# Kernel optimization log

Hardware: AMD Instinct MI355X
Metric: run time of the kernel (lower is better)

Reference implementation:

```python
import jax, jax.numpy as jnp
import numpy as np

S, B, C = 7, 2, 1
LAMBDA_COORD, LAMBDA_NOOBJ = 5.0, 0.5
EPS = 1e-6
BATCH = 32768


def setup_inputs() -> dict:
    key = jax.random.key(0)
    k1, k2, k3, k4 = jax.random.split(key, 4)
    predictions = jax.random.normal(k1, (BATCH, S, S, B * 5 + C), dtype=jnp.float32)
    coords = jax.random.uniform(k2, (BATCH, S, S, 4), dtype=jnp.float32) * 0.9 + 0.05
    conf = jax.random.randint(k3, (BATCH, S, S, 1), 0, 2).astype(jnp.float32)  # exactly 0 or 1
    cls = jax.random.randint(k4, (BATCH, S, S, C), 0, 2).astype(jnp.float32)
    targets = jnp.concatenate([coords, conf, cls], axis=-1)  # [BATCH,S,S,6]
    return {"predictions": predictions, "targets": targets}


def reference(predictions, targets):
    dt = predictions.dtype
    obj = (targets[..., 4] == 1.0).astype(dt)      # [bs,S,S]
    noobj = (targets[..., 4] == 0.0).astype(dt)    # [bs,S,S]

    pb = predictions[..., : B * 5].reshape(predictions.shape[:-1] + (B, 5))  # [bs,S,S,B,5]
    tb = targets[..., :5]                                                    # [bs,S,S,5]

    # IoU of each of the B predicted boxes vs the target box (per cell)
    sxy = jax.nn.sigmoid(pb[..., 0:2])
    awh = jnp.abs(pb[..., 2:4])
    p1 = sxy - awh / 2
    p2 = sxy + awh / 2
    t1 = tb[..., 0:2] - tb[..., 2:4] / 2
    t2 = tb[..., 0:2] + tb[..., 2:4] / 2
    lo = jnp.maximum(p1, t1[..., None, :])
    hi = jnp.minimum(p2, t2[..., None, :])
    inter = jnp.prod(jnp.maximum(hi - lo, 0.0), axis=-1)        # [bs,S,S,B]
    parea = jnp.prod(jnp.abs(p2 - p1), axis=-1)                 # [bs,S,S,B]
    tarea = (tb[..., 2] * tb[..., 3])[..., None]
    iou = inter / (parea + tarea - inter + EPS)

    best = jnp.argmax(iou, axis=-1)                             # [bs,S,S]
    bb = jnp.take_along_axis(pb, best[..., None, None], axis=-2)[..., 0, :]  # [bs,S,S,5]

    coord = LAMBDA_COORD * jnp.sum(
        obj * jnp.sum((jax.nn.sigmoid(bb[..., 0:2]) - tb[..., 0:2]) ** 2, axis=-1)
    )
    coord = coord + LAMBDA_COORD * jnp.sum(
        obj * jnp.sum((jnp.sqrt(jnp.abs(bb[..., 2:4]) + EPS) - jnp.sqrt(tb[..., 2:4] + EPS)) ** 2, axis=-1)
    )

    conf_obj = jnp.sum(obj * (jax.nn.sigmoid(bb[..., 4]) - tb[..., 4]) ** 2)

    conf_noobj = LAMBDA_NOOBJ * jnp.sum(
        noobj[..., None] * (jax.nn.sigmoid(pb[..., 4]) - tb[..., 4:5]) ** 2
    )

    # C == 1: binary cross-entropy with logits, summed over obj cells
    pc = predictions[..., B * 5 : B * 5 + C]
    tc = targets[..., 5 : 5 + C]
    bce = jnp.maximum(pc, 0.0) - pc * tc + jnp.log1p(jnp.exp(-jnp.abs(pc)))
    class_loss = jnp.sum(obj[..., None] * bce)

    bs = predictions.shape[0]
    total = (coord + conf_obj + conf_noobj + class_loss) / bs
    return (total, coord / bs, conf_obj / bs, conf_noobj / bs, class_loss / bs)
```

## Files before the change

kernel.cpp:

```cpp
#include <hip/hip_runtime.h>
#include <math.h>


#define PRED_C 11
#define TGT_C  6
#define TPB    256
#define CELLS_PER_THREAD 2
#define LAMBDA_COORD 5.0f
#define LAMBDA_NOOBJ 0.5f
#define EPSV 1e-6f

typedef float f4u __attribute__((ext_vector_type(4), aligned(4)));
typedef float f2u __attribute__((ext_vector_type(2), aligned(4)));

__device__ __forceinline__ float fsig(float x) {
    return __builtin_amdgcn_rcpf(1.0f + __expf(-x));
}

__device__ __forceinline__ void cell_loss(f4u a, f4u b, f4u c, f4u t4, f2u t2,
                                          float& acc_coord, float& acc_cobj,
                                          float& acc_cnoobj, float& acc_cls)
{
    const float tx = t4.x, ty = t4.y, tw = t4.z, th = t4.w;
    const float tconf = t2.x, tcls = t2.y;
    const float obj   = (tconf == 1.0f) ? 1.0f : 0.0f;
    const float noobj = (tconf == 0.0f) ? 1.0f : 0.0f;

    const float t1x = tx - tw * 0.5f, t1y = ty - th * 0.5f;
    const float t2x = tx + tw * 0.5f, t2y = ty + th * 0.5f;
    const float tarea = tw * th;

    const float px[2] = { a.x, b.y };
    const float py[2] = { a.y, b.z };
    const float pw[2] = { a.z, b.w };
    const float ph[2] = { a.w, c.y };
    const float pf[2] = { b.x, c.z };

    float iou[2], sx[2], sy[2], aw[2], ah[2], scf[2];
    #pragma unroll
    for (int bb = 0; bb < 2; ++bb) {
        sx[bb]  = fsig(px[bb]);
        sy[bb]  = fsig(py[bb]);
        scf[bb] = fsig(pf[bb]);
        aw[bb]  = fabsf(pw[bb]);
        ah[bb]  = fabsf(ph[bb]);
        const float p1x = sx[bb] - aw[bb] * 0.5f, p1y = sy[bb] - ah[bb] * 0.5f;
        const float p2x = sx[bb] + aw[bb] * 0.5f, p2y = sy[bb] + ah[bb] * 0.5f;
        const float ix = fminf(p2x, t2x) - fmaxf(p1x, t1x);
        const float iy = fminf(p2y, t2y) - fmaxf(p1y, t1y);
        const float inter = fmaxf(ix, 0.0f) * fmaxf(iy, 0.0f);
        const float parea = aw[bb] * ah[bb];
        iou[bb] = inter * __builtin_amdgcn_rcpf(parea + tarea - inter + EPSV);
    }
    const int best = (iou[1] > iou[0]) ? 1 : 0;

    const float dx = sx[best] - tx;
    const float dy = sy[best] - ty;
    const float dw = __builtin_amdgcn_sqrtf(aw[best] + EPSV) -
                     __builtin_amdgcn_sqrtf(tw + EPSV);
    const float dh = __builtin_amdgcn_sqrtf(ah[best] + EPSV) -
                     __builtin_amdgcn_sqrtf(th + EPSV);
    acc_coord += LAMBDA_COORD * obj * ((dx * dx + dy * dy) + (dw * dw + dh * dh));

    const float sc = scf[best];
    acc_cobj += obj * (sc - tconf) * (sc - tconf);

    const float d0 = scf[0] - tconf;
    const float d1 = scf[1] - tconf;
    acc_cnoobj += LAMBDA_NOOBJ * noobj * (d0 * d0 + d1 * d1);

    const float pc = c.w;
    const float bce = fmaxf(pc, 0.0f) - pc * tcls +
                      __logf(1.0f + __expf(-fabsf(pc)));
    acc_cls += obj * bce;
}

__global__ __launch_bounds__(TPB) void yolo_partial_kernel(
    const float* __restrict__ pred,
    const float* __restrict__ tgt,
    float* __restrict__ partials)
{
    __shared__ float red[4][4];
    const int tid = threadIdx.x;
    const long long c0 = (long long)blockIdx.x * (TPB * CELLS_PER_THREAD) + tid;
    const long long c1 = c0 + TPB;

    const float* p0 = pred + c0 * PRED_C;
    const float* p1 = pred + c1 * PRED_C;
    const float* t0 = tgt  + c0 * TGT_C;
    const float* t1 = tgt  + c1 * TGT_C;

    const f4u a0 = *(const f4u*)(p0);
    const f4u b0 = *(const f4u*)(p0 + 4);
    const f4u cc0 = *(const f4u*)(p0 + 7);
    const f4u a1 = *(const f4u*)(p1);
    const f4u b1 = *(const f4u*)(p1 + 4);
    const f4u cc1 = *(const f4u*)(p1 + 7);
    const f4u t40 = *(const f4u*)(t0);
    const f2u t20 = *(const f2u*)(t0 + 4);
    const f4u t41 = *(const f4u*)(t1);
    const f2u t21 = *(const f2u*)(t1 + 4);

    float coord = 0.f, cobj = 0.f, cnoobj = 0.f, cls = 0.f;
    cell_loss(a0, b0, cc0, t40, t20, coord, cobj, cnoobj, cls);
    cell_loss(a1, b1, cc1, t41, t21, coord, cobj, cnoobj, cls);

    #pragma unroll
    for (int off = 32; off >= 1; off >>= 1) {
        coord  += __shfl_down(coord, off);
        cobj   += __shfl_down(cobj, off);
        cnoobj += __shfl_down(cnoobj, off);
        cls    += __shfl_down(cls, off);
    }
    const int wave = tid >> 6;
    const int lane = tid & 63;
    if (lane == 0) {
        red[wave][0] = coord;
        red[wave][1] = cobj;
        red[wave][2] = cnoobj;
        red[wave][3] = cls;
    }
    __syncthreads();
    if (tid == 0) {
        float4 v;
        v.x = red[0][0] + red[1][0] + red[2][0] + red[3][0];
        v.y = red[0][1] + red[1][1] + red[2][1] + red[3][1];
        v.z = red[0][2] + red[1][2] + red[2][2] + red[3][2];
        v.w = red[0][3] + red[1][3] + red[2][3] + red[3][3];
        ((float4*)partials)[blockIdx.x] = v;
    }
}

__global__ __launch_bounds__(1024) void yolo_final_kernel(
    const float* __restrict__ partials,
    float* __restrict__ out,
    int nblk,
    float inv_bs)
{
    __shared__ float red[16][4];
    const int tid = threadIdx.x;

    float c = 0.f, co = 0.f, cn = 0.f, cl = 0.f;
    for (int i = tid; i < nblk; i += 1024) {
        const float4 v = ((const float4*)partials)[i];
        c += v.x; co += v.y; cn += v.z; cl += v.w;
    }
    #pragma unroll
    for (int off = 32; off >= 1; off >>= 1) {
        c  += __shfl_down(c, off);
        co += __shfl_down(co, off);
        cn += __shfl_down(cn, off);
        cl += __shfl_down(cl, off);
    }
    const int wave = tid >> 6;
    const int lane = tid & 63;
    if (lane == 0) {
        red[wave][0] = c;
        red[wave][1] = co;
        red[wave][2] = cn;
        red[wave][3] = cl;
    }
    __syncthreads();
    if (tid == 0) {
        float sc = 0.f, sco = 0.f, scn = 0.f, scl = 0.f;
        #pragma unroll
        for (int w = 0; w < 16; ++w) {
            sc  += red[w][0];
            sco += red[w][1];
            scn += red[w][2];
            scl += red[w][3];
        }
        out[0] = (sc + sco + scn + scl) * inv_bs;
        out[1] = sc  * inv_bs;
        out[2] = sco * inv_bs;
        out[3] = scn * inv_bs;
        out[4] = scl * inv_bs;
    }
}

extern "C" void kernel_launch(void* const* d_in, const int* in_sizes, int n_in,
                              void* d_out, int out_size, void* d_ws, size_t ws_size,
                              hipStream_t stream) {
    const float* pred = (const float*)d_in[0];
    const float* tgt  = (const float*)d_in[1];
    float* out = (float*)d_out;
    float* partials = (float*)d_ws;

    const long long batch = (long long)in_sizes[0] / (7 * 7 * PRED_C);
    const long long cells = batch * 49;
    const int nblk = (int)(cells / (TPB * CELLS_PER_THREAD));

    yolo_partial_kernel<<<nblk, TPB, 0, stream>>>(pred, tgt, partials);
    yolo_final_kernel<<<1, 1024, 0, stream>>>(partials, out, nblk,
                                              1.0f / (float)batch);
}
```

Baseline: 130.7 us.

## Stage cell data through LDS with direct global-to-LDS loads

Each block now copies its contiguous slice of predictions and targets into shared memory using coalesced 16-byte global_load_lds transfers, then computes cells from LDS. Cells per thread double from two to four, so the grid has half as many blocks. The aim is to replace the strided, unaligned per-thread vector loads with fully coalesced streaming. In exchange, each block uses about 68 KB of LDS, which limits occupancy, and reads at stride 11 from LDS may cause bank conflicts.

```diff
diff --git a/kernel.cpp b/kernel.cpp
--- a/kernel.cpp
+++ b/kernel.cpp
@@ -5,24 +5,32 @@
 #define PRED_C 11
 #define TGT_C  6
 #define TPB    256
-#define CELLS_PER_THREAD 2
+#define CPT    4
+#define CPB    (TPB * CPT)
+#define PRED_F (CPB * PRED_C)
+#define TGT_F  (CPB * TGT_C)
 #define LAMBDA_COORD 5.0f
 #define LAMBDA_NOOBJ 0.5f
 #define EPSV 1e-6f
 
-typedef float f4u __attribute__((ext_vector_type(4), aligned(4)));
-typedef float f2u __attribute__((ext_vector_type(2), aligned(4)));
-
 __device__ __forceinline__ float fsig(float x) {
     return __builtin_amdgcn_rcpf(1.0f + __expf(-x));
 }
 
-__device__ __forceinline__ void cell_loss(f4u a, f4u b, f4u c, f4u t4, f2u t2,
+__device__ __forceinline__ void gload_lds16(const float* g, float* l) {
+    __builtin_amdgcn_global_load_lds(
+        (const __attribute__((address_space(1))) void*)g,
+        (__attribute__((address_space(3))) void*)l,
+        16, 0, 0);
+}
+
+__device__ __forceinline__ void cell_loss(const float* __restrict__ p,
+                                          const float* __restrict__ t,
                                           float& acc_coord, float& acc_cobj,
                                           float& acc_cnoobj, float& acc_cls)
 {
-    const float tx = t4.x, ty = t4.y, tw = t4.z, th = t4.w;
-    const float tconf = t2.x, tcls = t2.y;
+    const float tx = t[0], ty = t[1], tw = t[2], th = t[3];
+    const float tconf = t[4], tcls = t[5];
     const float obj   = (tconf == 1.0f) ? 1.0f : 0.0f;
     const float noobj = (tconf == 0.0f) ? 1.0f : 0.0f;
 
@@ -30,11 +38,11 @@
     const float t2x = tx + tw * 0.5f, t2y = ty + th * 0.5f;
     const float tarea = tw * th;
 
-    const float px[2] = { a.x, b.y };
-    const float py[2] = { a.y, b.z };
-    const float pw[2] = { a.z, b.w };
-    const float ph[2] = { a.w, c.y };
-    const float pf[2] = { b.x, c.z };
+    const float px[2] = { p[0], p[5] };
+    const float py[2] = { p[1], p[6] };
+    const float pw[2] = { p[2], p[7] };
+    const float ph[2] = { p[3], p[8] };
+    const float pf[2] = { p[4], p[9] };
 
     float iou[2], sx[2], sy[2], aw[2], ah[2], scf[2];
     #pragma unroll
@@ -69,7 +77,7 @@
     const float d1 = scf[1] - tconf;
     acc_cnoobj += LAMBDA_NOOBJ * noobj * (d0 * d0 + d1 * d1);
 
-    const float pc = c.w;
+    const float pc = p[10];
     const float bce = fmaxf(pc, 0.0f) - pc * tcls +
                       __logf(1.0f + __expf(-fabsf(pc)));
     acc_cls += obj * bce;
@@ -80,30 +88,38 @@
     const float* __restrict__ tgt,
     float* __restrict__ partials)
 {
+    __shared__ __align__(16) float smem[PRED_F + TGT_F];
     __shared__ float red[4][4];
-    const int tid = threadIdx.x;
-    const long long c0 = (long long)blockIdx.x * (TPB * CELLS_PER_THREAD) + tid;
-    const long long c1 = c0 + TPB;
-
-    const float* p0 = pred + c0 * PRED_C;
-    const float* p1 = pred + c1 * PRED_C;
-    const float* t0 = tgt  + c0 * TGT_C;
-    const float* t1 = tgt  + c1 * TGT_C;
-
-    const f4u a0 = *(const f4u*)(p0);
-    const f4u b0 = *(const f4u*)(p0 + 4);
-    const f4u cc0 = *(const f4u*)(p0 + 7);
-    const f4u a1 = *(const f4u*)(p1);
-    const f4u b1 = *(const f4u*)(p1 + 4);
-    const f4u cc1 = *(const f4u*)(p1 + 7);
-    const f4u t40 = *(const f4u*)(t0);
-    const f2u t20 = *(const f2u*)(t0 + 4);
-    const f4u t41 = *(const f4u*)(t1);
-    const f2u t21 = *(const f2u*)(t1 + 4);
+    float* spred = smem;
+    float* stgt  = smem + PRED_F;
+
+    const int tid  = threadIdx.x;
+    const int wave = tid >> 6;
+    const int lane = tid & 63;
+
+    const size_t blk = blockIdx.x;
+    const float* gp = pred + blk * (size_t)PRED_F + (size_t)wave * 256 + (size_t)lane * 4;
+    const float* gt = tgt  + blk * (size_t)TGT_F  + (size_t)wave * 256 + (size_t)lane * 4;
+    float* lp = spred + wave * 256;
+    float* lt = stgt  + wave * 256;
+
+    #pragma unroll
+    for (int i = 0; i < PRED_C; ++i)
+        gload_lds16(gp + i * 1024, lp + i * 1024);
+    #pragma unroll
+    for (int i = 0; i < TGT_C; ++i)
+        gload_lds16(gt + i * 1024, lt + i * 1024);
+
+    asm volatile("s_waitcnt vmcnt(0)" ::: "memory");
+    __syncthreads();
 
     float coord = 0.f, cobj = 0.f, cnoobj = 0.f, cls = 0.f;
-    cell_loss(a0, b0, cc0, t40, t20, coord, cobj, cnoobj, cls);
-    cell_loss(a1, b1, cc1, t41, t21, coord, cobj, cnoobj, cls);
+    #pragma unroll
+    for (int k = 0; k < CPT; ++k) {
+        const int cell = tid + k * TPB;
+        cell_loss(spred + cell * PRED_C, stgt + cell * TGT_C,
+                  coord, cobj, cnoobj, cls);
+    }
 
     #pragma unroll
     for (int off = 32; off >= 1; off >>= 1) {
@@ -112,8 +128,6 @@
         cnoobj += __shfl_down(cnoobj, off);
         cls    += __shfl_down(cls, off);
     }
-    const int wave = tid >> 6;
-    const int lane = tid & 63;
     if (lane == 0) {
         red[wave][0] = coord;
         red[wave][1] = cobj;
@@ -188,7 +202,7 @@
 
     const long long batch = (long long)in_sizes[0] / (7 * 7 * PRED_C);
     const long long cells = batch * 49;
-    const int nblk = (int)(cells / (TPB * CELLS_PER_THREAD));
+    const int nblk = (int)(cells / CPB);
 
     yolo_partial_kernel<<<nblk, TPB, 0, stream>>>(pred, tgt, partials);
     yolo_final_kernel<<<1, 1024, 0, stream>>>(partials, out, nblk,
```

Result: no change. 132.1 us (+1.0%).
